# Kernel tuning notes

Hardware: AMD Instinct MI355X
Metric: run time of the kernel (lower is better)

The kernel has to match this reference:

```python
import jax, jax.numpy as jnp
import numpy as np
from jax import lax

DN = ('NCHW', 'OIHW', 'NCHW')
EPS_BN = 1e-5
EPS_NORM = 1e-8
THRESH = 0.5


def _conv(x, w, b, p):
    y = lax.conv_general_dilated(x, w, (1, 1), [(p, p), (p, p)], dimension_numbers=DN)
    return y + b[None, :, None, None]


def _bn(x, g, be, m, v):
    # inference-mode BatchNorm2d using running stats
    inv = g * lax.rsqrt(v + EPS_BN)
    return x * inv[None, :, None, None] + (be - m * inv)[None, :, None, None]


def _lrelu(x):
    return jnp.where(x >= 0, x, 0.01 * x)


def _cnn(x, p):
    # Convlayer: residual conv stack, 1 -> 16 -> 32 -> 32 -> 1 channels
    residual = x
    x = _lrelu(_bn(_conv(x, p['w1'], p['b1'], 1), p['g1'], p['be1'], p['m1'], p['v1']))
    x = _lrelu(_bn(_conv(x, p['w2'], p['b2'], 1), p['g2'], p['be2'], p['m2'], p['v2']))
    x = _lrelu(_bn(_conv(x, p['w3'], p['b3'], 2), p['g3'], p['be3'], p['m3'], p['v3']))
    x = _bn(_conv(x, p['w4'], p['b4'], 1), p['g4'], p['be4'], p['m4'], p['v4'])
    return _lrelu(x + residual)


def _make_params(key):
    ks = jax.random.split(key, 32)
    ki = iter(ks)
    def w(shape, fan_in):
        return jax.random.normal(next(ki), shape, jnp.float32) * (1.0 / np.sqrt(fan_in))
    def bn(c):
        return (1.0 + 0.1 * jax.random.normal(next(ki), (c,), jnp.float32),
                0.1 * jax.random.normal(next(ki), (c,), jnp.float32),
                0.1 * jax.random.normal(next(ki), (c,), jnp.float32),
                0.5 + jax.random.uniform(next(ki), (c,), jnp.float32))
    p = {}
    p['w0'] = w((1, 3, 3, 3), 27); p['b0'] = jnp.zeros((1,), jnp.float32)
    p['w1'] = w((16, 1, 3, 3), 9); p['b1'] = jnp.zeros((16,), jnp.float32)
    p['g1'], p['be1'], p['m1'], p['v1'] = bn(16)
    p['w2'] = w((32, 16, 3, 3), 144); p['b2'] = jnp.zeros((32,), jnp.float32)
    p['g2'], p['be2'], p['m2'], p['v2'] = bn(32)
    p['w3'] = w((32, 32, 5, 5), 800); p['b3'] = jnp.zeros((32,), jnp.float32)
    p['g3'], p['be3'], p['m3'], p['v3'] = bn(32)
    p['w4'] = w((1, 32, 3, 3), 288); p['b4'] = jnp.zeros((1,), jnp.float32)
    p['g4'], p['be4'], p['m4'], p['v4'] = bn(1)
    return p


def setup_inputs() -> dict:
    key = jax.random.key(0)
    k_gt, k_refs, k_p = jax.random.split(key, 3)
    B, R, H, W = 8, 4, 256, 256
    inp = {
        'gt': jax.random.normal(k_gt, (B, 3, H, W), jnp.float32),
        'refs': jax.random.normal(k_refs, (B, R, 1, H, W), jnp.float32),
    }
    inp.update(_make_params(k_p))
    return inp


def reference(gt, refs,
              w0, b0,
              w1, b1, g1, be1, m1, v1,
              w2, b2, g2, be2, m2, v2,
              w3, b3, g3, be3, m3, v3,
              w4, b4, g4, be4, m4, v4):
    p = dict(w1=w1, b1=b1, g1=g1, be1=be1, m1=m1, v1=v1,
             w2=w2, b2=b2, g2=g2, be2=be2, m2=m2, v2=v2,
             w3=w3, b3=b3, g3=g3, be3=be3, m3=m3, v3=v3,
             w4=w4, b4=b4, g4=g4, be4=be4, m4=m4, v4=v4)
    B, R, _, H, W = refs.shape
    gt1 = _conv(gt, w0, b0, 1)                 # [B,1,H,W]
    gt_feat = _cnn(gt1, p)                     # [B,1,H,W]
    refs_feat = _cnn(refs.reshape(B * R, 1, H, W), p).reshape(B, R, 1, H, W)
    diff_maps = jnp.abs(gt_feat[:, None] - refs_feat)          # [B,R,1,H,W]
    total = diff_maps.sum(axis=2)                              # [B,R,H,W]
    mn = total.min(axis=1, keepdims=True)
    mx = total.max(axis=1, keepdims=True)
    norm = jnp.clip((total - mn) / (mx - mn + EPS_NORM), 0.1, 1.0)
    dissim_map = jnp.where(norm > THRESH, norm, jnp.zeros_like(norm))  # [B,R,H,W]
    ref_idx = jnp.argmax(dissim_map, axis=1)[:, None]          # [B,1,H,W]
    # collage loop == gather of refs_feat along the ref axis
    collage = jnp.take_along_axis(refs_feat[:, :, 0], ref_idx, axis=1)  # [B,1,H,W]
    return dissim_map, collage
```

## Files before the change

### kernel.cpp

```cpp
#include <hip/hip_runtime.h>
#include <math.h>

#define HW 256
#define NPIX 65536

__device__ __forceinline__ float lrelu(float x) { return x >= 0.f ? x : 0.01f * x; }

__global__ __launch_bounds__(256) void conv0_kernel(const float* __restrict__ gt,
                                                    const float* __restrict__ w0,
                                                    const float* __restrict__ b0,
                                                    float* __restrict__ gt1) {
  int idx = blockIdx.x * 256 + threadIdx.x;
  int n = idx >> 16;
  int px = idx & 65535;
  int y = px >> 8, x = px & 255;
  float acc = b0[0];
  #pragma unroll
  for (int c = 0; c < 3; ++c) {
    const float* src = gt + (size_t)(n * 3 + c) * NPIX;
    #pragma unroll
    for (int ky = 0; ky < 3; ++ky) {
      int yy = y + ky - 1;
      if (yy < 0 || yy > 255) continue;
      #pragma unroll
      for (int kx = 0; kx < 3; ++kx) {
        int xx = x + kx - 1;
        if (xx < 0 || xx > 255) continue;
        acc = fmaf(src[yy * HW + xx], w0[(c * 3 + ky) * 3 + kx], acc);
      }
    }
  }
  gt1[idx] = acc;
}

__global__ __launch_bounds__(256) void conv1_kernel(const float* __restrict__ gt1,
                                                    const float* __restrict__ refs,
                                                    const float* __restrict__ w1,
                                                    const float* __restrict__ b1,
                                                    const float* __restrict__ g1,
                                                    const float* __restrict__ be1,
                                                    const float* __restrict__ m1,
                                                    const float* __restrict__ v1,
                                                    float* __restrict__ out, int i0) {
  __shared__ float sIn[34 * 34];
  __shared__ float sW[144];
  __shared__ float sScale[16], sShift[16];
  const int t = threadIdx.x;
  const int nz = blockIdx.z, n = i0 + nz;
  const int X0 = blockIdx.x * 32, Y0 = blockIdx.y * 32;
  const float* src = (n < 8) ? (gt1 + (size_t)n * NPIX) : (refs + (size_t)(n - 8) * NPIX);
  for (int id = t; id < 34 * 34; id += 256) {
    int row = id / 34, col = id - row * 34;
    int gy = Y0 + row - 1, gx = X0 + col - 1;
    float val = 0.f;
    if (gy >= 0 && gy < HW && gx >= 0 && gx < HW) val = src[gy * HW + gx];
    sIn[id] = val;
  }
  if (t < 144) sW[t] = w1[t];
  if (t < 16) {
    float inv = g1[t] / sqrtf(v1[t] + 1e-5f);
    sScale[t] = inv;
    sShift[t] = b1[t] * inv + be1[t] - m1[t] * inv;
  }
  __syncthreads();
  const int tx = t & 15, ty = t >> 4;
  const int lx = tx * 2, ly = ty * 2;
  float rin[4][4];
  #pragma unroll
  for (int r = 0; r < 4; ++r)
    #pragma unroll
    for (int c = 0; c < 4; ++c) rin[r][c] = sIn[(ly + r) * 34 + lx + c];
  #pragma unroll
  for (int oc = 0; oc < 16; ++oc) {
    float wv[9];
    #pragma unroll
    for (int k = 0; k < 9; ++k) wv[k] = sW[oc * 9 + k];
    float a[2][2] = {{0.f, 0.f}, {0.f, 0.f}};
    #pragma unroll
    for (int ky = 0; ky < 3; ++ky)
      #pragma unroll
      for (int kx = 0; kx < 3; ++kx) {
        const float wc = wv[ky * 3 + kx];
        a[0][0] = fmaf(rin[ky][kx], wc, a[0][0]);
        a[0][1] = fmaf(rin[ky][kx + 1], wc, a[0][1]);
        a[1][0] = fmaf(rin[ky + 1][kx], wc, a[1][0]);
        a[1][1] = fmaf(rin[ky + 1][kx + 1], wc, a[1][1]);
      }
    const float sc = sScale[oc], sh = sShift[oc];
    #pragma unroll
    for (int dy = 0; dy < 2; ++dy)
      #pragma unroll
      for (int dx = 0; dx < 2; ++dx) {
        int gy = Y0 + ly + dy, gx = X0 + lx + dx;
        out[(size_t)(nz * 16 + oc) * NPIX + gy * HW + gx] = lrelu(a[dy][dx] * sc + sh);
      }
  }
}

template <int CIN, int K>
__global__ __launch_bounds__(256, 2) void convT5_kernel(const float* __restrict__ in,
                                                        const float* __restrict__ w,
                                                        const float* __restrict__ bias,
                                                        const float* __restrict__ gg,
                                                        const float* __restrict__ be,
                                                        const float* __restrict__ mm,
                                                        const float* __restrict__ vv_,
                                                        float* __restrict__ out) {
  constexpr int KK = K * K;
  constexpr int PAD = K / 2;
  constexpr int ROWS = 16 + K - 1;
  constexpr int NIN = ROWS * 36;
  constexpr int NQ = (NIN + 255) / 256;
  constexpr int RR = 2 + K - 1;
  __shared__ float sIn[2][NIN];
  __shared__ float sScale[32], sShift[32];
  const int t = threadIdx.x;
  if (t < 32) {
    float inv = gg[t] / sqrtf(vv_[t] + 1e-5f);
    sScale[t] = inv;
    sShift[t] = bias[t] * inv + be[t] - mm[t] * inv;
  }
  const int X0 = blockIdx.x * 32, Y0 = blockIdx.y * 16;
  const int nz = blockIdx.z;
  const int wave = __builtin_amdgcn_readfirstlane(t >> 6);
  const int lane = t & 63;
  const int x0l = (lane & 7) * 4, y0l = (lane >> 3) * 2;
  const int oc0 = wave * 8;
  const float* inN = in + (size_t)nz * CIN * NPIX;
  const float* wb = w + (size_t)oc0 * CIN * KK;

  int soff[NQ];
  bool svalid[NQ];
  #pragma unroll
  for (int q = 0; q < NQ; ++q) {
    int id = t + q * 256;
    int row = id / 36, col = id - row * 36;
    int gy = Y0 + row - PAD, gx = X0 + col - PAD;
    svalid[q] = (id < NIN) && gy >= 0 && gy < HW && gx >= 0 && gx < HW && (col < 32 + 2 * PAD);
    soff[q] = gy * HW + gx;
  }

  float acc[8][2][4];
  #pragma unroll
  for (int j = 0; j < 8; ++j)
    #pragma unroll
    for (int py = 0; py < 2; ++py)
      #pragma unroll
      for (int px = 0; px < 4; ++px) acc[j][py][px] = 0.f;

  float vi[NQ];
  #pragma unroll
  for (int q = 0; q < NQ; ++q) vi[q] = svalid[q] ? inN[soff[q]] : 0.f;
  #pragma unroll
  for (int q = 0; q < NQ; ++q) {
    int id = t + q * 256;
    if (id < NIN) sIn[0][id] = vi[q];
  }
  if (CIN > 1) {
    #pragma unroll
    for (int q = 0; q < NQ; ++q) vi[q] = svalid[q] ? inN[NPIX + soff[q]] : 0.f;
  }
  __syncthreads();

  for (int ic = 0; ic < CIN; ++ic) {
    const int cur = ic & 1;
    if (ic + 1 < CIN) {
      float* sNxt = sIn[cur ^ 1];
      #pragma unroll
      for (int q = 0; q < NQ; ++q) {
        int id = t + q * 256;
        if (id < NIN) sNxt[id] = vi[q];
      }
    }
    if (ic + 2 < CIN) {
      const float* src = inN + (size_t)(ic + 2) * NPIX;
      #pragma unroll
      for (int q = 0; q < NQ; ++q) vi[q] = svalid[q] ? src[soff[q]] : 0.f;
    }
    const float* sBase = sIn[cur];
    float rin[RR][8];
    #pragma unroll
    for (int r = 0; r < RR; ++r) {
      const float4 a4 = *reinterpret_cast<const float4*>(&sBase[(y0l + r) * 36 + x0l]);
      const float4 b4 = *reinterpret_cast<const float4*>(&sBase[(y0l + r) * 36 + x0l + 4]);
      rin[r][0] = a4.x; rin[r][1] = a4.y; rin[r][2] = a4.z; rin[r][3] = a4.w;
      rin[r][4] = b4.x; rin[r][5] = b4.y; rin[r][6] = b4.z; rin[r][7] = b4.w;
    }
    #pragma unroll
    for (int j = 0; j < 8; ++j) {
      const float* wp = wb + ((size_t)j * CIN + ic) * KK;
      float wr[KK];
      #pragma unroll
      for (int k = 0; k < KK; ++k) wr[k] = wp[k];
      #pragma unroll
      for (int ky = 0; ky < K; ++ky)
        #pragma unroll
        for (int kx = 0; kx < K; ++kx) {
          const float wc = wr[ky * K + kx];
          #pragma unroll
          for (int py = 0; py < 2; ++py)
            #pragma unroll
            for (int px = 0; px < 4; ++px)
              acc[j][py][px] = fmaf(rin[py + ky][px + kx], wc, acc[j][py][px]);
        }
    }
    __syncthreads();
  }

  float* outN = out + (size_t)nz * 32 * NPIX;
  #pragma unroll
  for (int j = 0; j < 8; ++j) {
    const float sc = sScale[oc0 + j], sh = sShift[oc0 + j];
    #pragma unroll
    for (int py = 0; py < 2; ++py) {
      float4 o;
      o.x = lrelu(acc[j][py][0] * sc + sh);
      o.y = lrelu(acc[j][py][1] * sc + sh);
      o.z = lrelu(acc[j][py][2] * sc + sh);
      o.w = lrelu(acc[j][py][3] * sc + sh);
      *reinterpret_cast<float4*>(
          &outN[(size_t)(oc0 + j) * NPIX + (Y0 + y0l + py) * HW + X0 + x0l]) = o;
    }
  }
}

__global__ __launch_bounds__(256) void conv4_kernel(const float* __restrict__ in,
                                                    const float* __restrict__ gt1,
                                                    const float* __restrict__ refs,
                                                    const float* __restrict__ w4,
                                                    const float* __restrict__ b4,
                                                    const float* __restrict__ g4,
                                                    const float* __restrict__ be4,
                                                    const float* __restrict__ m4,
                                                    const float* __restrict__ v4,
                                                    float* __restrict__ feat, int i0) {
  __shared__ float sIn[2][34 * 34];
  const int t = threadIdx.x;
  const int nz = blockIdx.z, n = i0 + nz;
  const int X0 = blockIdx.x * 32, Y0 = blockIdx.y * 32;
  const int tx = t & 15, ty = t >> 4;
  const int lx = tx * 2, ly = ty * 2;
  const float* inN = in + (size_t)nz * 32 * NPIX;

  int soff[5];
  bool svalid[5];
  #pragma unroll
  for (int q = 0; q < 5; ++q) {
    int id = t + q * 256;
    int row = id / 34, col = id - row * 34;
    int gy = Y0 + row - 1, gx = X0 + col - 1;
    svalid[q] = (id < 34 * 34) && gy >= 0 && gy < HW && gx >= 0 && gx < HW;
    soff[q] = gy * HW + gx;
  }

  float a[2][2] = {{0.f, 0.f}, {0.f, 0.f}};
  float vi[5];
  #pragma unroll
  for (int q = 0; q < 5; ++q) vi[q] = svalid[q] ? inN[soff[q]] : 0.f;
  #pragma unroll
  for (int q = 0; q < 5; ++q) {
    int id = t + q * 256;
    if (id < 34 * 34) sIn[0][id] = vi[q];
  }
  #pragma unroll
  for (int q = 0; q < 5; ++q) vi[q] = svalid[q] ? inN[NPIX + soff[q]] : 0.f;
  __syncthreads();

  int cur = 0;
  for (int ic = 0; ic < 32; ++ic) {
    const float* sBase = sIn[cur];
    float rin[4][4];
    #pragma unroll
    for (int r = 0; r < 4; ++r) {
      const float2 p0 = *reinterpret_cast<const float2*>(&sBase[(ly + r) * 34 + lx]);
      const float2 p1 = *reinterpret_cast<const float2*>(&sBase[(ly + r) * 34 + lx + 2]);
      rin[r][0] = p0.x; rin[r][1] = p0.y; rin[r][2] = p1.x; rin[r][3] = p1.y;
    }
    if (ic + 1 < 32) {
      float* sNxt = sIn[cur ^ 1];
      #pragma unroll
      for (int q = 0; q < 5; ++q) {
        int id = t + q * 256;
        if (id < 34 * 34) sNxt[id] = vi[q];
      }
    }
    if (ic + 2 < 32) {
      const float* src = inN + (size_t)(ic + 2) * NPIX;
      #pragma unroll
      for (int q = 0; q < 5; ++q) vi[q] = svalid[q] ? src[soff[q]] : 0.f;
    }
    const float* wp = w4 + ic * 9;
    float wv[9];
    #pragma unroll
    for (int k = 0; k < 9; ++k) wv[k] = wp[k];
    #pragma unroll
    for (int ky = 0; ky < 3; ++ky)
      #pragma unroll
      for (int kx = 0; kx < 3; ++kx) {
        const float wc = wv[ky * 3 + kx];
        a[0][0] = fmaf(rin[ky][kx], wc, a[0][0]);
        a[0][1] = fmaf(rin[ky][kx + 1], wc, a[0][1]);
        a[1][0] = fmaf(rin[ky + 1][kx], wc, a[1][0]);
        a[1][1] = fmaf(rin[ky + 1][kx + 1], wc, a[1][1]);
      }
    __syncthreads();
    cur ^= 1;
  }
  const float inv = g4[0] / sqrtf(v4[0] + 1e-5f);
  const float sh = b4[0] * inv + be4[0] - m4[0] * inv;
  const float* res = (n < 8) ? (gt1 + (size_t)n * NPIX) : (refs + (size_t)(n - 8) * NPIX);
  #pragma unroll
  for (int dy = 0; dy < 2; ++dy)
    #pragma unroll
    for (int dx = 0; dx < 2; ++dx) {
      int px = (Y0 + ly + dy) * HW + X0 + lx + dx;
      float val = a[dy][dx] * inv + sh + res[px];
      feat[(size_t)n * NPIX + px] = lrelu(val);
    }
}

__global__ __launch_bounds__(256) void final_kernel(const float* __restrict__ feat,
                                                    float* __restrict__ outD) {
  int idx = blockIdx.x * 256 + threadIdx.x;
  int b = idx >> 16, px = idx & 65535;
  float gv = feat[(size_t)b * NPIX + px];
  float tv[4];
  float mn = 1e30f, mx = -1e30f;
  #pragma unroll
  for (int r = 0; r < 4; ++r) {
    float rv = feat[(size_t)(8 + b * 4 + r) * NPIX + px];
    tv[r] = fabsf(gv - rv);
    mn = fminf(mn, tv[r]);
    mx = fmaxf(mx, tv[r]);
  }
  const float denom = mx - mn + 1e-8f;
  float d[4];
  #pragma unroll
  for (int r = 0; r < 4; ++r) {
    float nrm = (tv[r] - mn) / denom;
    nrm = fminf(fmaxf(nrm, 0.1f), 1.0f);
    d[r] = nrm > 0.5f ? nrm : 0.f;
    outD[(size_t)(b * 4 + r) * NPIX + px] = d[r];
  }
  int best = 0;
  float bv = d[0];
  #pragma unroll
  for (int r = 1; r < 4; ++r)
    if (d[r] > bv) { bv = d[r]; best = r; }
  outD[(size_t)32 * NPIX + (size_t)b * NPIX + px] =
      feat[(size_t)(8 + b * 4 + best) * NPIX + px];
}

extern "C" void kernel_launch(void* const* d_in, const int* in_sizes, int n_in,
                              void* d_out, int out_size, void* d_ws, size_t ws_size,
                              hipStream_t stream) {
  const float* gt   = (const float*)d_in[0];
  const float* refs = (const float*)d_in[1];
  const float* w0 = (const float*)d_in[2];
  const float* b0 = (const float*)d_in[3];
  const float* w1 = (const float*)d_in[4];
  const float* b1 = (const float*)d_in[5];
  const float* g1 = (const float*)d_in[6];
  const float* be1 = (const float*)d_in[7];
  const float* m1 = (const float*)d_in[8];
  const float* v1 = (const float*)d_in[9];
  const float* w2 = (const float*)d_in[10];
  const float* b2 = (const float*)d_in[11];
  const float* g2 = (const float*)d_in[12];
  const float* be2 = (const float*)d_in[13];
  const float* m2 = (const float*)d_in[14];
  const float* v2 = (const float*)d_in[15];
  const float* w3 = (const float*)d_in[16];
  const float* b3 = (const float*)d_in[17];
  const float* g3 = (const float*)d_in[18];
  const float* be3 = (const float*)d_in[19];
  const float* m3 = (const float*)d_in[20];
  const float* v3 = (const float*)d_in[21];
  const float* w4 = (const float*)d_in[22];
  const float* b4 = (const float*)d_in[23];
  const float* g4 = (const float*)d_in[24];
  const float* be4 = (const float*)d_in[25];
  const float* m4 = (const float*)d_in[26];
  const float* v4 = (const float*)d_in[27];

  float* ws = (float*)d_ws;
  float* gt1  = ws;
  float* feat = gt1 + (size_t)8 * NPIX;
  float* bufBase = feat + (size_t)40 * NPIX;

  size_t fixedBytes = (size_t)(8 + 40) * NPIX * sizeof(float);
  size_t avail = (ws_size > fixedBytes) ? (ws_size - fixedBytes) : 0;
  size_t perImg = (size_t)2 * 32 * NPIX * sizeof(float);
  int maxC = (int)(avail / perImg);
  static const int divs[8] = {40, 20, 10, 8, 5, 4, 2, 1};
  int chunk = 1;
  for (int i = 0; i < 8; ++i)
    if (divs[i] <= maxC) { chunk = divs[i]; break; }

  float* bufA = bufBase;
  float* bufB = bufA + (size_t)chunk * 32 * NPIX;

  conv0_kernel<<<2048, 256, 0, stream>>>(gt, w0, b0, gt1);

  for (int i0 = 0; i0 < 40; i0 += chunk) {
    conv1_kernel<<<dim3(8, 8, chunk), 256, 0, stream>>>(gt1, refs, w1, b1, g1, be1, m1, v1,
                                                        bufA, i0);
    convT5_kernel<16, 3><<<dim3(8, 16, chunk), 256, 0, stream>>>(bufA, w2, b2, g2, be2, m2, v2,
                                                                 bufB);
    convT5_kernel<32, 5><<<dim3(8, 16, chunk), 256, 0, stream>>>(bufB, w3, b3, g3, be3, m3, v3,
                                                                 bufA);
    conv4_kernel<<<dim3(8, 8, chunk), 256, 0, stream>>>(bufA, gt1, refs, w4, b4, g4, be4, m4,
                                                        v4, feat, i0);
  }

  final_kernel<<<2048, 256, 0, stream>>>(feat, (float*)d_out);
}
```

Measured before the change: 1.888 ms.

## Shrink conv tile to one output row per thread and raise occupancy

The templated 3x3/5x5 conv kernel now gives each thread 1x4 output pixels instead of 2x4 per channel, over an 8-row block tile instead of 16, doubling the grid in y. Input rows are streamed one kernel row at a time from shared memory, with a 40-float stride, rather than held in a register array, and weights are read per kernel row. Launch bounds are raised to target 8 blocks per SM. The aim is to cut register pressure and raise occupancy, at the cost of more halo reloads, more shared-memory reads per FMA, and less register reuse.

```diff
diff --git a/kernel.cpp b/kernel.cpp
--- a/kernel.cpp
+++ b/kernel.cpp
@@ -98,7 +98,7 @@
 }
 
 template <int CIN, int K>
-__global__ __launch_bounds__(256, 2) void convT5_kernel(const float* __restrict__ in,
+__global__ __launch_bounds__(256, 8) void convT6_kernel(const float* __restrict__ in,
                                                         const float* __restrict__ w,
                                                         const float* __restrict__ bias,
                                                         const float* __restrict__ gg,
@@ -108,10 +108,11 @@
                                                         float* __restrict__ out) {
   constexpr int KK = K * K;
   constexpr int PAD = K / 2;
-  constexpr int ROWS = 16 + K - 1;
-  constexpr int NIN = ROWS * 36;
+  constexpr int TROWS = 8 + K - 1;
+  constexpr int STRIDE = 40;
+  constexpr int COLS = 32 + 2 * PAD;
+  constexpr int NIN = TROWS * STRIDE;
   constexpr int NQ = (NIN + 255) / 256;
-  constexpr int RR = 2 + K - 1;
   __shared__ float sIn[2][NIN];
   __shared__ float sScale[32], sShift[32];
   const int t = threadIdx.x;
@@ -120,11 +121,12 @@
     sScale[t] = inv;
     sShift[t] = bias[t] * inv + be[t] - mm[t] * inv;
   }
-  const int X0 = blockIdx.x * 32, Y0 = blockIdx.y * 16;
+  const int X0 = blockIdx.x * 32, Y0 = blockIdx.y * 8;
   const int nz = blockIdx.z;
   const int wave = __builtin_amdgcn_readfirstlane(t >> 6);
   const int lane = t & 63;
-  const int x0l = (lane & 7) * 4, y0l = (lane >> 3) * 2;
+  const int x0l = (lane & 7) * 4;
+  const int yrow = lane >> 3;
   const int oc0 = wave * 8;
   const float* inN = in + (size_t)nz * CIN * NPIX;
   const float* wb = w + (size_t)oc0 * CIN * KK;
@@ -134,19 +136,17 @@
   #pragma unroll
   for (int q = 0; q < NQ; ++q) {
     int id = t + q * 256;
-    int row = id / 36, col = id - row * 36;
+    int row = id / STRIDE, col = id - row * STRIDE;
     int gy = Y0 + row - PAD, gx = X0 + col - PAD;
-    svalid[q] = (id < NIN) && gy >= 0 && gy < HW && gx >= 0 && gx < HW && (col < 32 + 2 * PAD);
+    svalid[q] = (id < NIN) && (col < COLS) && gy >= 0 && gy < HW && gx >= 0 && gx < HW;
     soff[q] = gy * HW + gx;
   }
 
-  float acc[8][2][4];
+  float acc[8][4];
   #pragma unroll
   for (int j = 0; j < 8; ++j)
     #pragma unroll
-    for (int py = 0; py < 2; ++py)
-      #pragma unroll
-      for (int px = 0; px < 4; ++px) acc[j][py][px] = 0.f;
+    for (int px = 0; px < 4; ++px) acc[j][px] = 0.f;
 
   float vi[NQ];
   #pragma unroll
@@ -178,49 +178,40 @@
       for (int q = 0; q < NQ; ++q) vi[q] = svalid[q] ? src[soff[q]] : 0.f;
     }
     const float* sBase = sIn[cur];
-    float rin[RR][8];
-    #pragma unroll
-    for (int r = 0; r < RR; ++r) {
-      const float4 a4 = *reinterpret_cast<const float4*>(&sBase[(y0l + r) * 36 + x0l]);
-      const float4 b4 = *reinterpret_cast<const float4*>(&sBase[(y0l + r) * 36 + x0l + 4]);
-      rin[r][0] = a4.x; rin[r][1] = a4.y; rin[r][2] = a4.z; rin[r][3] = a4.w;
-      rin[r][4] = b4.x; rin[r][5] = b4.y; rin[r][6] = b4.z; rin[r][7] = b4.w;
-    }
-    #pragma unroll
-    for (int j = 0; j < 8; ++j) {
-      const float* wp = wb + ((size_t)j * CIN + ic) * KK;
-      float wr[KK];
-      #pragma unroll
-      for (int k = 0; k < KK; ++k) wr[k] = wp[k];
-      #pragma unroll
-      for (int ky = 0; ky < K; ++ky)
+    #pragma unroll
+    for (int ky = 0; ky < K; ++ky) {
+      const float* rowp = &sBase[(yrow + ky) * STRIDE + x0l];
+      const float4 a4 = *reinterpret_cast<const float4*>(rowp);
+      const float4 b4 = *reinterpret_cast<const float4*>(rowp + 4);
+      float rin[8];
+      rin[0] = a4.x; rin[1] = a4.y; rin[2] = a4.z; rin[3] = a4.w;
+      rin[4] = b4.x; rin[5] = b4.y; rin[6] = b4.z; rin[7] = b4.w;
+      #pragma unroll
+      for (int j = 0; j < 8; ++j) {
+        const float* wp = wb + ((size_t)j * CIN + ic) * KK + ky * K;
         #pragma unroll
         for (int kx = 0; kx < K; ++kx) {
-          const float wc = wr[ky * K + kx];
+          const float wc = wp[kx];
           #pragma unroll
-          for (int py = 0; py < 2; ++py)
-            #pragma unroll
-            for (int px = 0; px < 4; ++px)
-              acc[j][py][px] = fmaf(rin[py + ky][px + kx], wc, acc[j][py][px]);
+          for (int px = 0; px < 4; ++px)
+            acc[j][px] = fmaf(rin[kx + px], wc, acc[j][px]);
         }
+      }
     }
     __syncthreads();
   }
 
   float* outN = out + (size_t)nz * 32 * NPIX;
+  const int orow = (Y0 + yrow) * HW + X0 + x0l;
   #pragma unroll
   for (int j = 0; j < 8; ++j) {
     const float sc = sScale[oc0 + j], sh = sShift[oc0 + j];
-    #pragma unroll
-    for (int py = 0; py < 2; ++py) {
-      float4 o;
-      o.x = lrelu(acc[j][py][0] * sc + sh);
-      o.y = lrelu(acc[j][py][1] * sc + sh);
-      o.z = lrelu(acc[j][py][2] * sc + sh);
-      o.w = lrelu(acc[j][py][3] * sc + sh);
-      *reinterpret_cast<float4*>(
-          &outN[(size_t)(oc0 + j) * NPIX + (Y0 + y0l + py) * HW + X0 + x0l]) = o;
-    }
+    float4 o;
+    o.x = lrelu(acc[j][0] * sc + sh);
+    o.y = lrelu(acc[j][1] * sc + sh);
+    o.z = lrelu(acc[j][2] * sc + sh);
+    o.w = lrelu(acc[j][3] * sc + sh);
+    *reinterpret_cast<float4*>(&outN[(size_t)(oc0 + j) * NPIX + orow]) = o;
   }
 }
 
@@ -405,9 +396,9 @@
   for (int i0 = 0; i0 < 40; i0 += chunk) {
     conv1_kernel<<<dim3(8, 8, chunk), 256, 0, stream>>>(gt1, refs, w1, b1, g1, be1, m1, v1,
                                                         bufA, i0);
-    convT5_kernel<16, 3><<<dim3(8, 16, chunk), 256, 0, stream>>>(bufA, w2, b2, g2, be2, m2, v2,
+    convT6_kernel<16, 3><<<dim3(8, 32, chunk), 256, 0, stream>>>(bufA, w2, b2, g2, be2, m2, v2,
                                                                  bufB);
-    convT5_kernel<32, 5><<<dim3(8, 16, chunk), 256, 0, stream>>>(bufB, w3, b3, g3, be3, m3, v3,
+    convT6_kernel<32, 5><<<dim3(8, 32, chunk), 256, 0, stream>>>(bufB, w3, b3, g3, be3, m3, v3,
                                                                  bufA);
     conv4_kernel<<<dim3(8, 8, chunk), 256, 0, stream>>>(bufA, gt1, refs, w4, b4, g4, be4, m4,
                                                         v4, feat, i0);
```

Measured after the change: 4.182 ms. 122% more time.
